# Optimization experiments

Measured on AMD Instinct MI355X. Metric: run time of the kernel, lower is better.

Reference implementation:

```python
import jax, jax.numpy as jnp
import numpy as np
from jax import lax

B_, L_ = 2, 512
D_MODEL, EXPAND, HEAD_DIM, NGROUPS, D_STATE, D_CONV = 512, 2, 64, 1, 64, 3
D_INNER = EXPAND * D_MODEL            # 1024
NHEADS = D_INNER // HEAD_DIM          # 16
CONV_DIM = D_INNER + 2 * NGROUPS * D_STATE   # 1152
D_IN_PROJ = 2 * D_INNER + 2 * NGROUPS * D_STATE + NHEADS  # 2192
RMS_EPS = 1e-5


def silu(x):
    return x * jax.nn.sigmoid(x)


def segsum(x):
    # x: (..., T) -> (..., T, T); out[..., i, j] = sum_{j<k<=i} x[..., k], -inf above diag
    T = x.shape[-1]
    xr = jnp.broadcast_to(x[..., None], x.shape + (T,))
    keep = jnp.tril(jnp.ones((T, T), dtype=bool), -1)
    xr = jnp.where(keep, xr, 0.0)
    s = jnp.cumsum(xr, axis=-2)
    diag = jnp.tril(jnp.ones((T, T), dtype=bool), 0)
    return jnp.where(diag, s, -jnp.inf)


def ssd(x, A, Bm, Cm, chunk):
    # x: (b,l,h,p), A: (b,l,h), Bm/Cm: (b,l,g,n); chunk==1 as in the source forward
    b, l, h, p = x.shape
    c = l // chunk
    n = Bm.shape[-1]
    x = x.reshape(b, c, chunk, h, p)
    Bm = Bm.reshape(b, c, chunk, Bm.shape[2], n)
    Cm = Cm.reshape(b, c, chunk, Cm.shape[2], n)
    A = A.reshape(b, c, chunk, h).transpose(0, 3, 1, 2)        # (b,h,c,l)
    A_cumsum = jnp.cumsum(A, axis=-1)
    Lmat = jnp.exp(segsum(A))                                   # (b,h,c,l,l)
    # broadcast group dim (g==1) to heads, matching torch.einsum broadcasting
    Bb = jnp.broadcast_to(Bm, (b, c, chunk, h, n))
    Cb = jnp.broadcast_to(Cm, (b, c, chunk, h, n))
    Y_diag = jnp.einsum('bclhn,bcshn,bhcls,bcshp->bclhp', Cb, Bb, Lmat, x)
    decay_states = jnp.exp(A_cumsum[:, :, :, -1:] - A_cumsum)   # (b,h,c,l)
    states = jnp.einsum('bclhn,bhcl,bclhp->bchpn', Bb, decay_states, x)
    states = jnp.concatenate([jnp.zeros_like(states[:, :1]), states], axis=1)  # (b,c+1,h,p,n)
    A_last = jnp.pad(A_cumsum[:, :, :, -1], ((0, 0), (0, 0), (1, 0)))          # (b,h,c+1)
    decay_chunk = jnp.exp(segsum(A_last))                       # (b,h,c+1,c+1)
    new_states = jnp.einsum('bhzc,bchpn->bzhpn', decay_chunk, states)
    states = new_states[:, :-1]                                 # (b,c,h,p,n)
    state_decay_out = jnp.exp(A_cumsum)
    Y_off = jnp.einsum('bclhn,bchpn,bhcl->bclhp', Cb, states, state_decay_out)
    return (Y_diag + Y_off).reshape(b, l, h, p)


def causal_dwconv(x, w, bias):
    # x: (B,L,C); w: (C,K) depthwise; torch pads (K-1) both sides then slices [:L] == left-pad only
    xt = x.transpose(0, 2, 1)
    y = lax.conv_general_dilated(xt, w[:, None, :], (1,), [(D_CONV - 1, 0)],
                                 feature_group_count=CONV_DIM,
                                 dimension_numbers=('NCH', 'OIH', 'NCH'))
    return y.transpose(0, 2, 1) + bias


def setup_inputs() -> dict:
    key = jax.random.key(0)
    ks = jax.random.split(key, 8)
    u = jax.random.normal(ks[0], (B_, L_, D_MODEL), dtype=jnp.float32)
    W_in = jax.random.normal(ks[1], (D_MODEL, D_IN_PROJ), dtype=jnp.float32) / np.sqrt(D_MODEL).astype(np.float32)
    conv_w = jax.random.normal(ks[2], (CONV_DIM, D_CONV), dtype=jnp.float32) * 0.3
    conv_b = jnp.zeros((CONV_DIM,), dtype=jnp.float32)
    dt = jnp.exp(jax.random.uniform(ks[3], (NHEADS,), dtype=jnp.float32)
                 * (np.float32(np.log(0.1)) - np.float32(np.log(0.001))) + np.float32(np.log(0.001)))
    dt = jnp.clip(dt, 1e-4, None)
    dt_bias = dt + jnp.log(-jnp.expm1(-dt))
    A_log = jnp.log(jax.random.uniform(ks[4], (NHEADS,), dtype=jnp.float32, minval=1.0, maxval=16.0))
    D_param = jnp.ones((NHEADS,), dtype=jnp.float32)
    rms_w = jnp.ones((D_INNER,), dtype=jnp.float32)
    W_out = jax.random.normal(ks[5], (D_INNER, D_MODEL), dtype=jnp.float32) / np.sqrt(D_INNER).astype(np.float32)
    return {"u": u, "W_in": W_in, "conv_w": conv_w, "conv_b": conv_b, "dt_bias": dt_bias,
            "A_log": A_log, "D_param": D_param, "rms_w": rms_w, "W_out": W_out}


def reference(u, W_in, conv_w, conv_b, dt_bias, A_log, D_param, rms_w, W_out):
    b, l, _ = u.shape
    zxbcdt = u @ W_in                                   # (b,l,D_IN_PROJ)
    z = zxbcdt[..., :D_INNER]
    xBC = zxbcdt[..., D_INNER:D_INNER + CONV_DIM]
    dt = zxbcdt[..., D_INNER + CONV_DIM:]
    dt = jax.nn.softplus(dt + dt_bias)                  # (b,l,h)
    A = -jnp.exp(A_log)                                 # (h,)
    xBC = silu(causal_dwconv(xBC, conv_w, conv_b))      # (b,l,CONV_DIM)
    x = xBC[..., :D_INNER].reshape(b, l, NHEADS, HEAD_DIM)
    Bm = xBC[..., D_INNER:D_INNER + D_STATE][:, :, None, :]     # (b,l,1,n)
    Cm = xBC[..., D_INNER + D_STATE:][:, :, None, :]            # (b,l,1,n)
    y = ssd(x * dt[..., None], A * dt, Bm, Cm, 1)       # (b,l,h,p)
    y = y + x * D_param[:, None]
    y = y.reshape(b, l, D_INNER)
    # gated RMSNorm
    yz = y * silu(z)
    y = yz * lax.rsqrt(jnp.mean(yz * yz, axis=-1, keepdims=True) + RMS_EPS) * rms_w
    return y @ W_out
```

## Files before the change

kernel.cpp:

```cpp
#include <hip/hip_runtime.h>
#include <hip/hip_bf16.h>

#define B_SZ 2
#define L_SZ 512
#define D_MODEL 512
#define D_INNER 1024
#define HEAD_DIM 64
#define NHEADS 16
#define D_STATE 64
#define D_CONV 3
#define CONV_DIM 1152
#define D_IN_PROJ 2192
#define BL (B_SZ * L_SZ)
#define RMS_EPS 1e-5f
#define QC 64
#define NCH 8
#define NPAD1 2304
#define PB 72

typedef __attribute__((ext_vector_type(8))) short short8t;
typedef __attribute__((ext_vector_type(8))) unsigned short ushort8t;
typedef __attribute__((ext_vector_type(4))) unsigned short ushort4t;
typedef __attribute__((ext_vector_type(4))) float f32x4;

__device__ __forceinline__ unsigned short f2bf(float f) {
    unsigned u = __float_as_uint(f);
    u += 0x7fff + ((u >> 16) & 1);
    return (unsigned short)(u >> 16);
}
__device__ __forceinline__ float bf2f(unsigned short u) {
    return __uint_as_float(((unsigned)u) << 16);
}

__device__ __forceinline__ void gload_lds16(const void* g, void* lds) {
    __builtin_amdgcn_global_load_lds(
        (const __attribute__((address_space(1))) unsigned int*)g,
        (__attribute__((address_space(3))) unsigned int*)lds, 16, 0, 0);
}

__device__ __forceinline__ void transpose_tile_bf16(const float* __restrict__ src,
                                                    const float* __restrict__ scale,
                                                    unsigned short* __restrict__ dst,
                                                    int K, int Nin, int tile, int ntn) {
    __shared__ float T[64][65];
    int tid = threadIdx.x;
    int nt = tile % ntn, kt = tile / ntn;
    int n0 = nt * 64, k0 = kt * 64;
#pragma unroll
    for (int rr = 0; rr < 4; ++rr) {
        int k = k0 + (tid >> 4) + rr * 16;
        float sc = scale ? scale[k] : 1.f;
        int nn = (tid & 15) * 4;
#pragma unroll
        for (int q = 0; q < 4; ++q) {
            int n = n0 + nn + q;
            T[(tid >> 4) + rr * 16][nn + q] = (n < Nin) ? src[(size_t)k * Nin + n] * sc : 0.f;
        }
    }
    __syncthreads();
    int nn2 = tid >> 2, kc = tid & 3;
    unsigned short ov[16];
#pragma unroll
    for (int j = 0; j < 16; ++j) ov[j] = f2bf(T[kc * 16 + j][nn2]);
    unsigned short* p = dst + (size_t)(n0 + nn2) * K + k0 + kc * 16;
    *(ushort8t*)p = *(ushort8t*)&ov[0];
    *(ushort8t*)(p + 8) = *(ushort8t*)&ov[8];
}

__global__ __launch_bounds__(256) void prep_kernel(const float* __restrict__ W_in,
                                                   const float* __restrict__ W_out,
                                                   const float* __restrict__ rms_w,
                                                   const float* __restrict__ u,
                                                   unsigned short* __restrict__ Wt1,
                                                   unsigned short* __restrict__ Wt2,
                                                   unsigned short* __restrict__ u_bf) {
    int bid = blockIdx.x;
    if (bid < 288) {
        transpose_tile_bf16(W_in, nullptr, Wt1, D_MODEL, D_IN_PROJ, bid, 36);
    } else if (bid < 416) {
        transpose_tile_bf16(W_out, rms_w, Wt2, D_INNER, D_MODEL, bid - 288, 8);
    } else {
        int i = ((bid - 416) * 256 + threadIdx.x) * 8;
        float4 v0 = *(const float4*)(u + i);
        float4 v1 = *(const float4*)(u + i + 4);
        unsigned short ov[8] = {f2bf(v0.x), f2bf(v0.y), f2bf(v0.z), f2bf(v0.w),
                                f2bf(v1.x), f2bf(v1.y), f2bf(v1.z), f2bf(v1.w)};
        *(ushort8t*)(u_bf + i) = *(ushort8t*)&ov[0];
    }
}

__global__ __launch_bounds__(256) void gemm_in(const unsigned short* __restrict__ A,
                                               const unsigned short* __restrict__ Bt,
                                               unsigned short* __restrict__ z_bf,
                                               unsigned short* __restrict__ xbc,
                                               float* __restrict__ dtb) {
    const int K = D_MODEL;
    __shared__ char sm[49152];
    int tid = threadIdx.x;
    int w = tid >> 6, l = tid & 63;
    int m0 = blockIdx.y * 64, n0 = blockIdx.x * 64;
    int wm = w >> 1, wn = w & 1;

    f32x4 acc[2][2];
#pragma unroll
    for (int i = 0; i < 2; ++i)
#pragma unroll
        for (int j = 0; j < 2; ++j) acc[i][j] = (f32x4){0.f, 0.f, 0.f, 0.f};

    auto stage = [&](const unsigned short* src, int row0, int k0, char* dst) {
#pragma unroll
        for (int p = 0; p < 2; ++p) {
            int c = w * 2 + p;
            int row = c * 8 + (l >> 3);
            int scb = ((l & 7) << 4) ^ ((row & 7) << 4);
            gload_lds16(src + (size_t)(row0 + row) * K + k0 + (scb >> 1), dst + c * 1024);
        }
    };

    const int nkt = K / 64;
    stage(A, m0, 0, sm);
    stage(Bt, n0, 0, sm + 8192);
    stage(A, m0, 64, sm + 16384);
    stage(Bt, n0, 64, sm + 16384 + 8192);

    for (int kt = 0; kt < nkt; ++kt) {
        if (kt + 2 < nkt) {
            char* d = sm + ((kt + 2) % 3) * 16384;
            stage(A, m0, (kt + 2) * 64, d);
            stage(Bt, n0, (kt + 2) * 64, d + 8192);
        }
        int inflight = nkt - 1 - kt;
        if (inflight >= 2)      asm volatile("s_waitcnt vmcnt(8)" ::: "memory");
        else if (inflight == 1) asm volatile("s_waitcnt vmcnt(4)" ::: "memory");
        else                    asm volatile("s_waitcnt vmcnt(0)" ::: "memory");
        __builtin_amdgcn_s_barrier();

        const char* Ab = sm + (kt % 3) * 16384;
        const char* Bb = Ab + 8192;
#pragma unroll
        for (int kk = 0; kk < 2; ++kk) {
            short8t af[2], bf[2];
#pragma unroll
            for (int i = 0; i < 2; ++i) {
                int r = wm * 32 + i * 16 + (l & 15);
                int cb = (kk * 64 + (l >> 4) * 16) ^ ((r & 7) << 4);
                af[i] = *(const short8t*)(Ab + r * 128 + cb);
            }
#pragma unroll
            for (int j = 0; j < 2; ++j) {
                int r = wn * 32 + j * 16 + (l & 15);
                int cb = (kk * 64 + (l >> 4) * 16) ^ ((r & 7) << 4);
                bf[j] = *(const short8t*)(Bb + r * 128 + cb);
            }
#pragma unroll
            for (int i = 0; i < 2; ++i)
#pragma unroll
                for (int j = 0; j < 2; ++j)
                    acc[i][j] = __builtin_amdgcn_mfma_f32_16x16x32_bf16(af[i], bf[j], acc[i][j], 0, 0, 0);
        }
        __builtin_amdgcn_s_barrier();
    }

#pragma unroll
    for (int i = 0; i < 2; ++i)
#pragma unroll
        for (int j = 0; j < 2; ++j) {
            int row = m0 + wm * 32 + i * 16 + (l >> 4) * 4;
            int col = n0 + wn * 32 + j * 16 + (l & 15);
#pragma unroll
            for (int r = 0; r < 4; ++r) {
                float v = acc[i][j][r];
                int rr = row + r;
                if (col < D_INNER) {
                    z_bf[(size_t)rr * D_INNER + col] = f2bf(v);
                } else if (col < D_INNER + CONV_DIM) {
                    xbc[(size_t)rr * CONV_DIM + (col - D_INNER)] = f2bf(v);
                } else if (col < D_IN_PROJ) {
                    dtb[(size_t)rr * 16 + (col - D_INNER - CONV_DIM)] = v;
                }
            }
        }
}

__device__ __forceinline__ float4 conv4b(const unsigned short* __restrict__ xrow,
                                         int gl, int ch,
                                         const float* __restrict__ conv_w,
                                         const float* __restrict__ conv_b) {
    ushort4t u2 = *(const ushort4t*)(xrow + ch);
    ushort4t u1 = {0, 0, 0, 0}, u0 = {0, 0, 0, 0};
    if (gl >= 1) u1 = *(const ushort4t*)(xrow + ch - CONV_DIM);
    if (gl >= 2) u0 = *(const ushort4t*)(xrow + ch - 2 * CONV_DIM);
    float4 o;
    float a;
    a = conv_b[ch+0] + conv_w[(ch+0)*3]*bf2f(u0[0]) + conv_w[(ch+0)*3+1]*bf2f(u1[0]) + conv_w[(ch+0)*3+2]*bf2f(u2[0]);
    o.x = a / (1.f + __expf(-a));
    a = conv_b[ch+1] + conv_w[(ch+1)*3]*bf2f(u0[1]) + conv_w[(ch+1)*3+1]*bf2f(u1[1]) + conv_w[(ch+1)*3+2]*bf2f(u2[1]);
    o.y = a / (1.f + __expf(-a));
    a = conv_b[ch+2] + conv_w[(ch+2)*3]*bf2f(u0[2]) + conv_w[(ch+2)*3+1]*bf2f(u1[2]) + conv_w[(ch+2)*3+2]*bf2f(u2[2]);
    o.z = a / (1.f + __expf(-a));
    a = conv_b[ch+3] + conv_w[(ch+3)*3]*bf2f(u0[3]) + conv_w[(ch+3)*3+1]*bf2f(u1[3]) + conv_w[(ch+3)*3+2]*bf2f(u2[3]);
    o.w = a / (1.f + __expf(-a));
    return o;
}

__device__ __forceinline__ float silu(float z) { return z / (1.f + __expf(-z)); }

__global__ __launch_bounds__(256) void ssd_passA(const unsigned short* __restrict__ xbc,
                                                 const float* __restrict__ dtb,
                                                 const unsigned short* __restrict__ z_bf,
                                                 const float* __restrict__ conv_w,
                                                 const float* __restrict__ conv_b,
                                                 const float* __restrict__ dt_bias,
                                                 const float* __restrict__ A_log,
                                                 const float* __restrict__ D_param,
                                                 unsigned short* __restrict__ y_bf,
                                                 unsigned short* __restrict__ yz_bf,
                                                 float* __restrict__ psum,
                                                 unsigned short* __restrict__ Zbuf,
                                                 float* __restrict__ Ebuf) {
    int blk = blockIdx.x;
    int h = blk & 15;
    int c = (blk >> 4) & 7;
    int b = blk >> 7;
    int tid = threadIdx.x;

    __shared__ __align__(16) unsigned short Cs_bf[QC][PB];
    __shared__ __align__(16) unsigned short Bs_bf[QC][PB];
    __shared__ __align__(16) unsigned short XDT_bf[QC][PB];
    __shared__ __align__(16) unsigned short BTw_bf[QC][PB];
    __shared__ float csh[QC], dts[QC], wh[QC];
    __shared__ float sq_lds[QC][2];
#define PS_bf Cs_bf

    int bl0 = b * L_SZ + c * QC;

    if (tid < 64) {
        int t = tid;
        float draw = dtb[(size_t)(bl0 + t) * 16 + h];
        float dtv = draw + dt_bias[h];
        dtv = (dtv > 20.f) ? dtv : log1pf(expf(dtv));
        float A = -expf(A_log[h]);
        float cs = A * dtv;
#pragma unroll
        for (int off = 1; off < 64; off <<= 1) {
            float tmp = __shfl_up(cs, off);
            if (t >= off) cs += tmp;
        }
        float cs63 = __shfl(cs, 63);
        dts[t] = dtv;
        csh[t] = cs;
        wh[t] = __expf(cs63 - cs);
        Ebuf[(((size_t)(b * NHEADS + h) * NCH) + c) * QC + t] = __expf(cs);
    }

    int row16 = tid >> 4;
    int col4 = (tid & 15) * 4;
#pragma unroll
    for (int r = 0; r < 4; ++r) {
        int t = r * 16 + row16;
        int gl = c * QC + t;
        const unsigned short* xrow = xbc + (size_t)(bl0 + t) * CONV_DIM;
        float4 Bv = conv4b(xrow, gl, D_INNER + col4, conv_w, conv_b);
        float4 Cv = conv4b(xrow, gl, D_INNER + D_STATE + col4, conv_w, conv_b);
        ushort4t bq = {f2bf(Bv.x), f2bf(Bv.y), f2bf(Bv.z), f2bf(Bv.w)};
        ushort4t cq = {f2bf(Cv.x), f2bf(Cv.y), f2bf(Cv.z), f2bf(Cv.w)};
        *(ushort4t*)&Bs_bf[t][col4] = bq;
        *(ushort4t*)&Cs_bf[t][col4] = cq;
    }
    __syncthreads();

#pragma unroll
    for (int r = 0; r < 4; ++r) {
        int t = r * 16 + row16;
        int gl = c * QC + t;
        const unsigned short* xrow = xbc + (size_t)(bl0 + t) * CONV_DIM;
        float4 xv = conv4b(xrow, gl, h * HEAD_DIM + col4, conv_w, conv_b);
        float d = dts[t], wt = wh[t];
        xv.x *= d; xv.y *= d; xv.z *= d; xv.w *= d;
        ushort4t xq = {f2bf(xv.x), f2bf(xv.y), f2bf(xv.z), f2bf(xv.w)};
        ushort4t bq = *(ushort4t*)&Bs_bf[t][col4];
#pragma unroll
        for (int q = 0; q < 4; ++q) {
            int ch = col4 + q;
            int f8 = ((ch >> 2) & 7) << 3;
            XDT_bf[ch][t ^ f8] = xq[q];
            BTw_bf[ch][t ^ f8] = f2bf(bf2f(bq[q]) * wt);
        }
    }
    __syncthreads();

    int l = tid & 63, wv = tid >> 6;
    int wm = wv >> 1, wn = wv & 1;
    int fr = l & 15, fq = l >> 4;

    f32x4 g[2][2];
    {
#pragma unroll
        for (int i = 0; i < 2; ++i)
#pragma unroll
            for (int j = 0; j < 2; ++j) g[i][j] = (f32x4){0.f, 0.f, 0.f, 0.f};
#pragma unroll
        for (int kk = 0; kk < 2; ++kk) {
            short8t af[2], bb[2];
#pragma unroll
            for (int i = 0; i < 2; ++i)
                af[i] = *(const short8t*)&Cs_bf[wm * 32 + i * 16 + fr][kk * 32 + fq * 8];
#pragma unroll
            for (int j = 0; j < 2; ++j)
                bb[j] = *(const short8t*)&Bs_bf[wn * 32 + j * 16 + fr][kk * 32 + fq * 8];
#pragma unroll
            for (int i = 0; i < 2; ++i)
#pragma unroll
                for (int j = 0; j < 2; ++j)
                    g[i][j] = __builtin_amdgcn_mfma_f32_16x16x32_bf16(af[i], bb[j], g[i][j], 0, 0, 0);
        }
    }
    __syncthreads();

    {
#pragma unroll
        for (int i = 0; i < 2; ++i)
#pragma unroll
            for (int j = 0; j < 2; ++j) {
                int s = wn * 32 + j * 16 + fr;
                float css = csh[s];
#pragma unroll
                for (int r = 0; r < 4; ++r) {
                    int t = wm * 32 + i * 16 + fq * 4 + r;
                    float v = (s <= t) ? g[i][j][r] * __expf(csh[t] - css) : 0.f;
                    PS_bf[t][s] = f2bf(v);
                }
            }
    }
    __syncthreads();

    {
        f32x4 yv[2][2];
#pragma unroll
        for (int i = 0; i < 2; ++i)
#pragma unroll
            for (int j = 0; j < 2; ++j) yv[i][j] = (f32x4){0.f, 0.f, 0.f, 0.f};
#pragma unroll
        for (int kk = 0; kk < 2; ++kk) {
            short8t af[2], bb[2];
            int K0 = kk * 32 + fq * 8;
#pragma unroll
            for (int i = 0; i < 2; ++i)
                af[i] = *(const short8t*)&PS_bf[wm * 32 + i * 16 + fr][K0];
#pragma unroll
            for (int j = 0; j < 2; ++j) {
                int r = wn * 32 + j * 16 + fr;
                bb[j] = *(const short8t*)&XDT_bf[r][K0 ^ (((r >> 2) & 7) << 3)];
            }
#pragma unroll
            for (int i = 0; i < 2; ++i)
#pragma unroll
                for (int j = 0; j < 2; ++j)
                    yv[i][j] = __builtin_amdgcn_mfma_f32_16x16x32_bf16(af[i], bb[j], yv[i][j], 0, 0, 0);
        }
        float Dp = D_param[h];
        if (c == 0) {
            float sloc[2][4] = {{0.f, 0.f, 0.f, 0.f}, {0.f, 0.f, 0.f, 0.f}};
#pragma unroll
            for (int i = 0; i < 2; ++i)
#pragma unroll
                for (int j = 0; j < 2; ++j) {
                    int p = wn * 32 + j * 16 + fr;
                    int f8 = ((p >> 2) & 7) << 3;
#pragma unroll
                    for (int r = 0; r < 4; ++r) {
                        int t = wm * 32 + i * 16 + fq * 4 + r;
                        float xval = bf2f(XDT_bf[p][t ^ f8]);
                        float yval = yv[i][j][r] + (Dp / dts[t]) * xval;
                        float z = bf2f(z_bf[(size_t)(bl0 + t) * D_INNER + h * HEAD_DIM + p]);
                        float yz = yval * silu(z);
                        yz_bf[(size_t)(bl0 + t) * D_INNER + h * HEAD_DIM + p] = f2bf(yz);
                        sloc[i][r] += yz * yz;
                    }
                }
#pragma unroll
            for (int i = 0; i < 2; ++i)
#pragma unroll
                for (int r = 0; r < 4; ++r) {
                    float v = sloc[i][r];
                    v += __shfl_xor(v, 1); v += __shfl_xor(v, 2);
                    v += __shfl_xor(v, 4); v += __shfl_xor(v, 8);
                    if (fr == 0) {
                        int t = wm * 32 + i * 16 + fq * 4 + r;
                        sq_lds[t][wn] = v;
                    }
                }
            __syncthreads();
            if (tid < 64)
                psum[(size_t)(bl0 + tid) * 16 + h] = sq_lds[tid][0] + sq_lds[tid][1];
        } else {
#pragma unroll
            for (int i = 0; i < 2; ++i)
#pragma unroll
                for (int j = 0; j < 2; ++j) {
                    int p = wn * 32 + j * 16 + fr;
                    int f8 = ((p >> 2) & 7) << 3;
#pragma unroll
                    for (int r = 0; r < 4; ++r) {
                        int t = wm * 32 + i * 16 + fq * 4 + r;
                        float xval = bf2f(XDT_bf[p][t ^ f8]);
                        float fct = Dp / dts[t];
                        y_bf[(size_t)(bl0 + t) * D_INNER + h * HEAD_DIM + p] =
                            f2bf(yv[i][j][r] + fct * xval);
                    }
                }
        }
    }

    {
        f32x4 zv[2][2];
#pragma unroll
        for (int i = 0; i < 2; ++i)
#pragma unroll
            for (int j = 0; j < 2; ++j) zv[i][j] = (f32x4){0.f, 0.f, 0.f, 0.f};
#pragma unroll
        for (int kk = 0; kk < 2; ++kk) {
            short8t af[2], bb[2];
            int K0 = kk * 32 + fq * 8;
#pragma unroll
            for (int i = 0; i < 2; ++i) {
                int r = wm * 32 + i * 16 + fr;
                af[i] = *(const short8t*)&XDT_bf[r][K0 ^ (((r >> 2) & 7) << 3)];
            }
#pragma unroll
            for (int j = 0; j < 2; ++j) {
                int r = wn * 32 + j * 16 + fr;
                bb[j] = *(const short8t*)&BTw_bf[r][K0 ^ (((r >> 2) & 7) << 3)];
            }
#pragma unroll
            for (int i = 0; i < 2; ++i)
#pragma unroll
                for (int j = 0; j < 2; ++j)
                    zv[i][j] = __builtin_amdgcn_mfma_f32_16x16x32_bf16(af[i], bb[j], zv[i][j], 0, 0, 0);
        }
        unsigned short* Zr = Zbuf + (((size_t)(b * NHEADS + h) * NCH) + c) * (HEAD_DIM * D_STATE);
#pragma unroll
        for (int i = 0; i < 2; ++i)
#pragma unroll
            for (int j = 0; j < 2; ++j) {
                int n = wn * 32 + j * 16 + fr;
#pragma unroll
                for (int r = 0; r < 4; ++r) {
                    int p = wm * 32 + i * 16 + fq * 4 + r;
                    Zr[p * D_STATE + n] = f2bf(zv[i][j][r]);
                }
            }
    }
#undef PS_bf
}

__global__ __launch_bounds__(256) void ssd_passC(const unsigned short* __restrict__ xbc,
                                                 const unsigned short* __restrict__ z_bf,
                                                 const float* __restrict__ conv_w,
                                                 const float* __restrict__ conv_b,
                                                 const unsigned short* __restrict__ Zbuf,
                                                 const float* __restrict__ Ebuf,
                                                 const unsigned short* __restrict__ y_bf,
                                                 unsigned short* __restrict__ yz_bf,
                                                 float* __restrict__ psum) {
    int blk = blockIdx.x;
    int h = blk & 15;
    int q = blk >> 4;
    int c = 1 + (q % 7);
    int b = q / 7;
    int tid = threadIdx.x;

    __shared__ __align__(16) unsigned short Cs_bf[QC][PB];
    __shared__ __align__(16) unsigned short S_bf[QC][PB];
    __shared__ float Eh[QC];
    __shared__ float sq_lds[QC][2];

    int bl0 = b * L_SZ + c * QC;
    const unsigned short* Zb = Zbuf + ((size_t)(b * NHEADS + h) * NCH) * (HEAD_DIM * D_STATE);
    const float* Eb = Ebuf + ((size_t)(b * NHEADS + h) * NCH) * QC;

    {
        int p = tid >> 2, nq = (tid & 3) * 16;
        float S16[16];
#pragma unroll
        for (int qq = 0; qq < 16; ++qq) S16[qq] = 0.f;
        float wgt = 1.f;
        for (int j = c - 1; j >= 0; --j) {
            const unsigned short* Zj = Zb + (size_t)j * (HEAD_DIM * D_STATE) + p * D_STATE + nq;
            ushort8t za = *(const ushort8t*)Zj;
            ushort8t zb2 = *(const ushort8t*)(Zj + 8);
#pragma unroll
            for (int qq = 0; qq < 8; ++qq) {
                S16[qq] += wgt * bf2f(za[qq]);
                S16[8 + qq] += wgt * bf2f(zb2[qq]);
            }
            wgt *= Eb[(size_t)j * QC + 63];
        }
#pragma unroll
        for (int q4 = 0; q4 < 4; ++q4) {
            ushort4t s4 = {f2bf(S16[q4 * 4 + 0]), f2bf(S16[q4 * 4 + 1]),
                           f2bf(S16[q4 * 4 + 2]), f2bf(S16[q4 * 4 + 3])};
            *(ushort4t*)&S_bf[p][nq + q4 * 4] = s4;
        }
    }

    int row16 = tid >> 4, col4 = (tid & 15) * 4;
#pragma unroll
    for (int r = 0; r < 4; ++r) {
        int t = r * 16 + row16;
        int gl = c * QC + t;
        const unsigned short* xrow = xbc + (size_t)(bl0 + t) * CONV_DIM;
        float4 Cv = conv4b(xrow, gl, D_INNER + D_STATE + col4, conv_w, conv_b);
        ushort4t cq = {f2bf(Cv.x), f2bf(Cv.y), f2bf(Cv.z), f2bf(Cv.w)};
        *(ushort4t*)&Cs_bf[t][col4] = cq;
    }
    if (tid < 64)
        Eh[tid] = Ebuf[(((size_t)(b * NHEADS + h) * NCH) + c) * QC + tid];
    __syncthreads();

    int l = tid & 63, wv = tid >> 6;
    int wm = wv >> 1, wn = wv & 1;
    int fr = l & 15, fq = l >> 4;
    f32x4 acc[2][2];
#pragma unroll
    for (int i = 0; i < 2; ++i)
#pragma unroll
        for (int j = 0; j < 2; ++j) acc[i][j] = (f32x4){0.f, 0.f, 0.f, 0.f};
#pragma unroll
    for (int kk = 0; kk < 2; ++kk) {
        short8t af[2], bb[2];
#pragma unroll
        for (int i = 0; i < 2; ++i)
            af[i] = *(const short8t*)&Cs_bf[wm * 32 + i * 16 + fr][kk * 32 + fq * 8];
#pragma unroll
        for (int j = 0; j < 2; ++j)
            bb[j] = *(const short8t*)&S_bf[wn * 32 + j * 16 + fr][kk * 32 + fq * 8];
#pragma unroll
        for (int i = 0; i < 2; ++i)
#pragma unroll
            for (int j = 0; j < 2; ++j)
                acc[i][j] = __builtin_amdgcn_mfma_f32_16x16x32_bf16(af[i], bb[j], acc[i][j], 0, 0, 0);
    }

    float sloc[2][4] = {{0.f, 0.f, 0.f, 0.f}, {0.f, 0.f, 0.f, 0.f}};
#pragma unroll
    for (int i = 0; i < 2; ++i)
#pragma unroll
        for (int j = 0; j < 2; ++j) {
            int p = wn * 32 + j * 16 + fr;
#pragma unroll
            for (int r = 0; r < 4; ++r) {
                int t = wm * 32 + i * 16 + fq * 4 + r;
                size_t idx = (size_t)(bl0 + t) * D_INNER + h * HEAD_DIM + p;
                float yval = bf2f(y_bf[idx]) + Eh[t] * acc[i][j][r];
                float z = bf2f(z_bf[idx]);
                float yz = yval * silu(z);
                yz_bf[idx] = f2bf(yz);
                sloc[i][r] += yz * yz;
            }
        }
#pragma unroll
    for (int i = 0; i < 2; ++i)
#pragma unroll
        for (int r = 0; r < 4; ++r) {
            float v = sloc[i][r];
            v += __shfl_xor(v, 1); v += __shfl_xor(v, 2);
            v += __shfl_xor(v, 4); v += __shfl_xor(v, 8);
            if (fr == 0) {
                int t = wm * 32 + i * 16 + fq * 4 + r;
                sq_lds[t][wn] = v;
            }
        }
    __syncthreads();
    if (tid < 64)
        psum[(size_t)(bl0 + tid) * 16 + h] = sq_lds[tid][0] + sq_lds[tid][1];
}

__global__ __launch_bounds__(256) void gemm_out(const unsigned short* __restrict__ A,
                                                const unsigned short* __restrict__ Bt,
                                                const float* __restrict__ psum,
                                                float* __restrict__ C) {
    const int N = D_MODEL, K = D_INNER;
    __shared__ char sm[36864];
    __shared__ float scl[32];
    int tid = threadIdx.x;
    int w = tid >> 6, l = tid & 63;
    int m0 = blockIdx.y * 32, n0 = blockIdx.x * 64;
    int wm = w >> 1, wn = w & 1;

    f32x4 acc[2];
    acc[0] = (f32x4){0.f, 0.f, 0.f, 0.f};
    acc[1] = (f32x4){0.f, 0.f, 0.f, 0.f};

    auto stageA = [&](int k0, char* dst) {
        int row = w * 8 + (l >> 3);
        int scb = ((l & 7) << 4) ^ ((row & 7) << 4);
        gload_lds16(A + (size_t)(m0 + row) * K + k0 + (scb >> 1), dst + w * 1024);
    };
    auto stageB = [&](int k0, char* dst) {
#pragma unroll
        for (int p = 0; p < 2; ++p) {
            int c = w * 2 + p;
            int row = c * 8 + (l >> 3);
            int scb = ((l & 7) << 4) ^ ((row & 7) << 4);
            gload_lds16(Bt + (size_t)(n0 + row) * K + k0 + (scb >> 1), dst + c * 1024);
        }
    };

    const int nkt = K / 64;
    stageA(0, sm); stageB(0, sm + 4096);
    stageA(64, sm + 12288); stageB(64, sm + 12288 + 4096);

    for (int kt = 0; kt < nkt; ++kt) {
        if (kt + 2 < nkt) {
            char* d = sm + ((kt + 2) % 3) * 12288;
            stageA((kt + 2) * 64, d);
            stageB((kt + 2) * 64, d + 4096);
        }
        int inflight = nkt - 1 - kt;
        if (inflight >= 2)      asm volatile("s_waitcnt vmcnt(6)" ::: "memory");
        else if (inflight == 1) asm volatile("s_waitcnt vmcnt(3)" ::: "memory");
        else                    asm volatile("s_waitcnt vmcnt(0)" ::: "memory");
        __builtin_amdgcn_s_barrier();

        const char* Ab = sm + (kt % 3) * 12288;
        const char* Bb = Ab + 4096;
#pragma unroll
        for (int kk = 0; kk < 2; ++kk) {
            short8t af;
            {
                int r = wm * 16 + (l & 15);
                int cb = (kk * 64 + (l >> 4) * 16) ^ ((r & 7) << 4);
                af = *(const short8t*)(Ab + r * 128 + cb);
            }
#pragma unroll
            for (int j = 0; j < 2; ++j) {
                int r = wn * 32 + j * 16 + (l & 15);
                int cb = (kk * 64 + (l >> 4) * 16) ^ ((r & 7) << 4);
                short8t bfv = *(const short8t*)(Bb + r * 128 + cb);
                acc[j] = __builtin_amdgcn_mfma_f32_16x16x32_bf16(af, bfv, acc[j], 0, 0, 0);
            }
        }
        __builtin_amdgcn_s_barrier();
    }

    if (tid < 32) {
        const float* pr = psum + (size_t)(m0 + tid) * 16;
        float s = 0.f;
#pragma unroll
        for (int qq = 0; qq < 16; ++qq) s += pr[qq];
        scl[tid] = rsqrtf(s / (float)D_INNER + RMS_EPS);
    }
    __syncthreads();

#pragma unroll
    for (int j = 0; j < 2; ++j) {
        int col = n0 + wn * 32 + j * 16 + (l & 15);
        int rloc = wm * 16 + (l >> 4) * 4;
#pragma unroll
        for (int r = 0; r < 4; ++r)
            C[(size_t)(m0 + rloc + r) * N + col] = acc[j][r] * scl[rloc + r];
    }
}

extern "C" void kernel_launch(void* const* d_in, const int* in_sizes, int n_in,
                              void* d_out, int out_size, void* d_ws, size_t ws_size,
                              hipStream_t stream) {
    const float* u       = (const float*)d_in[0];
    const float* W_in    = (const float*)d_in[1];
    const float* conv_w  = (const float*)d_in[2];
    const float* conv_b  = (const float*)d_in[3];
    const float* dt_bias = (const float*)d_in[4];
    const float* A_log   = (const float*)d_in[5];
    const float* D_param = (const float*)d_in[6];
    const float* rms_w   = (const float*)d_in[7];
    const float* W_out   = (const float*)d_in[8];
    float* out = (float*)d_out;

    float* ws = (float*)d_ws;
    float* Ebuf = ws;
    float* dtb  = Ebuf + (size_t)32 * NCH * QC;
    float* psum = dtb + (size_t)BL * 16;
    unsigned short* u_bf  = (unsigned short*)(psum + (size_t)BL * 16);
    unsigned short* Wt1   = u_bf + (size_t)BL * D_MODEL;
    unsigned short* Wt2   = Wt1 + (size_t)NPAD1 * D_MODEL;
    unsigned short* xbc   = Wt2 + (size_t)D_MODEL * D_INNER;
    unsigned short* z_bf  = xbc + (size_t)BL * CONV_DIM;
    unsigned short* y_bf  = z_bf + (size_t)BL * D_INNER;
    unsigned short* yz_bf = y_bf + (size_t)BL * D_INNER;
    unsigned short* Zbuf  = yz_bf + (size_t)BL * D_INNER;

    prep_kernel<<<672, 256, 0, stream>>>(W_in, W_out, rms_w, u, Wt1, Wt2, u_bf);

    gemm_in<<<dim3(NPAD1 / 64, BL / 64), 256, 0, stream>>>(
        u_bf, Wt1, z_bf, xbc, dtb);

    ssd_passA<<<B_SZ * NCH * NHEADS, 256, 0, stream>>>(
        xbc, dtb, z_bf, conv_w, conv_b, dt_bias, A_log, D_param,
        y_bf, yz_bf, psum, Zbuf, Ebuf);
    ssd_passC<<<224, 256, 0, stream>>>(
        xbc, z_bf, conv_w, conv_b, Zbuf, Ebuf, y_bf, yz_bf, psum);

    gemm_out<<<dim3(D_MODEL / 64, BL / 32), 256, 0, stream>>>(
        yz_bf, Wt2, psum, out);
}
```

Before: 46.25 us.

## Fuse SSD passes into one kernel with inter-block flag synchronization

Merges ssd_passA and ssd_passC into a single kernel. Each chunk block publishes its chunk state (Zbuf) and chunk decay, then sets a release flag. Later chunks spin on acquire flags of earlier chunks and add the inter-chunk contribution directly in registers. This removes a kernel launch, the y_bf round trip through global memory and the recomputed B/C conv in passC. The cost is a spin-wait dependency that assumes all 256 blocks are co-resident and serializes later chunks behind earlier ones.

```diff
diff --git a/kernel.cpp b/kernel.cpp
--- a/kernel.cpp
+++ b/kernel.cpp
@@ -73,8 +73,10 @@
                                                    const float* __restrict__ u,
                                                    unsigned short* __restrict__ Wt1,
                                                    unsigned short* __restrict__ Wt2,
-                                                   unsigned short* __restrict__ u_bf) {
+                                                   unsigned short* __restrict__ u_bf,
+                                                   unsigned* __restrict__ flags) {
     int bid = blockIdx.x;
+    if (bid == 0) flags[threadIdx.x] = 0u;
     if (bid < 288) {
         transpose_tile_bf16(W_in, nullptr, Wt1, D_MODEL, D_IN_PROJ, bid, 36);
     } else if (bid < 416) {
@@ -205,7 +207,7 @@
 
 __device__ __forceinline__ float silu(float z) { return z / (1.f + __expf(-z)); }
 
-__global__ __launch_bounds__(256) void ssd_passA(const unsigned short* __restrict__ xbc,
+__global__ __launch_bounds__(256) void ssd_fused(const unsigned short* __restrict__ xbc,
                                                  const float* __restrict__ dtb,
                                                  const unsigned short* __restrict__ z_bf,
                                                  const float* __restrict__ conv_w,
@@ -213,15 +215,16 @@
                                                  const float* __restrict__ dt_bias,
                                                  const float* __restrict__ A_log,
                                                  const float* __restrict__ D_param,
-                                                 unsigned short* __restrict__ y_bf,
                                                  unsigned short* __restrict__ yz_bf,
                                                  float* __restrict__ psum,
                                                  unsigned short* __restrict__ Zbuf,
-                                                 float* __restrict__ Ebuf) {
+                                                 float* __restrict__ dec,
+                                                 unsigned* __restrict__ flags) {
     int blk = blockIdx.x;
     int h = blk & 15;
     int c = (blk >> 4) & 7;
     int b = blk >> 7;
+    int bh = b * NHEADS + h;
     int tid = threadIdx.x;
 
     __shared__ __align__(16) unsigned short Cs_bf[QC][PB];
@@ -230,7 +233,8 @@
     __shared__ __align__(16) unsigned short BTw_bf[QC][PB];
     __shared__ float csh[QC], dts[QC], wh[QC];
     __shared__ float sq_lds[QC][2];
-#define PS_bf Cs_bf
+#define P_bf Bs_bf
+#define S_bf BTw_bf
 
     int bl0 = b * L_SZ + c * QC;
 
@@ -250,7 +254,7 @@
         dts[t] = dtv;
         csh[t] = cs;
         wh[t] = __expf(cs63 - cs);
-        Ebuf[(((size_t)(b * NHEADS + h) * NCH) + c) * QC + t] = __expf(cs);
+        if (t == 0) dec[bh * NCH + c] = __expf(cs63);
     }
 
     int row16 = tid >> 4;
@@ -294,135 +298,77 @@
     int fr = l & 15, fq = l >> 4;
 
     f32x4 g[2][2];
+#pragma unroll
+    for (int i = 0; i < 2; ++i)
+#pragma unroll
+        for (int j = 0; j < 2; ++j) g[i][j] = (f32x4){0.f, 0.f, 0.f, 0.f};
+#pragma unroll
+    for (int kk = 0; kk < 2; ++kk) {
+        short8t af[2], bb[2];
+#pragma unroll
+        for (int i = 0; i < 2; ++i)
+            af[i] = *(const short8t*)&Cs_bf[wm * 32 + i * 16 + fr][kk * 32 + fq * 8];
+#pragma unroll
+        for (int j = 0; j < 2; ++j)
+            bb[j] = *(const short8t*)&Bs_bf[wn * 32 + j * 16 + fr][kk * 32 + fq * 8];
+#pragma unroll
+        for (int i = 0; i < 2; ++i)
+#pragma unroll
+            for (int j = 0; j < 2; ++j)
+                g[i][j] = __builtin_amdgcn_mfma_f32_16x16x32_bf16(af[i], bb[j], g[i][j], 0, 0, 0);
+    }
+    __syncthreads();
+
+#pragma unroll
+    for (int i = 0; i < 2; ++i)
+#pragma unroll
+        for (int j = 0; j < 2; ++j) {
+            int s = wn * 32 + j * 16 + fr;
+            float css = csh[s];
+#pragma unroll
+            for (int r = 0; r < 4; ++r) {
+                int t = wm * 32 + i * 16 + fq * 4 + r;
+                float v = (s <= t) ? g[i][j][r] * __expf(csh[t] - css) : 0.f;
+                P_bf[t][s] = f2bf(v);
+            }
+        }
+    __syncthreads();
+
+    f32x4 yv[2][2];
+#pragma unroll
+    for (int i = 0; i < 2; ++i)
+#pragma unroll
+        for (int j = 0; j < 2; ++j) yv[i][j] = (f32x4){0.f, 0.f, 0.f, 0.f};
+#pragma unroll
+    for (int kk = 0; kk < 2; ++kk) {
+        short8t af[2], bb[2];
+        int K0 = kk * 32 + fq * 8;
+#pragma unroll
+        for (int i = 0; i < 2; ++i)
+            af[i] = *(const short8t*)&P_bf[wm * 32 + i * 16 + fr][K0];
+#pragma unroll
+        for (int j = 0; j < 2; ++j) {
+            int r = wn * 32 + j * 16 + fr;
+            bb[j] = *(const short8t*)&XDT_bf[r][K0 ^ (((r >> 2) & 7) << 3)];
+        }
+#pragma unroll
+        for (int i = 0; i < 2; ++i)
+#pragma unroll
+            for (int j = 0; j < 2; ++j)
+                yv[i][j] = __builtin_amdgcn_mfma_f32_16x16x32_bf16(af[i], bb[j], yv[i][j], 0, 0, 0);
+    }
+
     {
-#pragma unroll
-        for (int i = 0; i < 2; ++i)
-#pragma unroll
-            for (int j = 0; j < 2; ++j) g[i][j] = (f32x4){0.f, 0.f, 0.f, 0.f};
-#pragma unroll
-        for (int kk = 0; kk < 2; ++kk) {
-            short8t af[2], bb[2];
-#pragma unroll
-            for (int i = 0; i < 2; ++i)
-                af[i] = *(const short8t*)&Cs_bf[wm * 32 + i * 16 + fr][kk * 32 + fq * 8];
-#pragma unroll
-            for (int j = 0; j < 2; ++j)
-                bb[j] = *(const short8t*)&Bs_bf[wn * 32 + j * 16 + fr][kk * 32 + fq * 8];
-#pragma unroll
-            for (int i = 0; i < 2; ++i)
-#pragma unroll
-                for (int j = 0; j < 2; ++j)
-                    g[i][j] = __builtin_amdgcn_mfma_f32_16x16x32_bf16(af[i], bb[j], g[i][j], 0, 0, 0);
-        }
-    }
-    __syncthreads();
-
-    {
-#pragma unroll
-        for (int i = 0; i < 2; ++i)
-#pragma unroll
-            for (int j = 0; j < 2; ++j) {
-                int s = wn * 32 + j * 16 + fr;
-                float css = csh[s];
-#pragma unroll
-                for (int r = 0; r < 4; ++r) {
-                    int t = wm * 32 + i * 16 + fq * 4 + r;
-                    float v = (s <= t) ? g[i][j][r] * __expf(csh[t] - css) : 0.f;
-                    PS_bf[t][s] = f2bf(v);
-                }
-            }
-    }
-    __syncthreads();
-
-    {
-        f32x4 yv[2][2];
-#pragma unroll
-        for (int i = 0; i < 2; ++i)
-#pragma unroll
-            for (int j = 0; j < 2; ++j) yv[i][j] = (f32x4){0.f, 0.f, 0.f, 0.f};
+        f32x4 zv[2][2];
+#pragma unroll
+        for (int i = 0; i < 2; ++i)
+#pragma unroll
+            for (int j = 0; j < 2; ++j) zv[i][j] = (f32x4){0.f, 0.f, 0.f, 0.f};
 #pragma unroll
         for (int kk = 0; kk < 2; ++kk) {
             short8t af[2], bb[2];
             int K0 = kk * 32 + fq * 8;
 #pragma unroll
-            for (int i = 0; i < 2; ++i)
-                af[i] = *(const short8t*)&PS_bf[wm * 32 + i * 16 + fr][K0];
-#pragma unroll
-            for (int j = 0; j < 2; ++j) {
-                int r = wn * 32 + j * 16 + fr;
-                bb[j] = *(const short8t*)&XDT_bf[r][K0 ^ (((r >> 2) & 7) << 3)];
-            }
-#pragma unroll
-            for (int i = 0; i < 2; ++i)
-#pragma unroll
-                for (int j = 0; j < 2; ++j)
-                    yv[i][j] = __builtin_amdgcn_mfma_f32_16x16x32_bf16(af[i], bb[j], yv[i][j], 0, 0, 0);
-        }
-        float Dp = D_param[h];
-        if (c == 0) {
-            float sloc[2][4] = {{0.f, 0.f, 0.f, 0.f}, {0.f, 0.f, 0.f, 0.f}};
-#pragma unroll
-            for (int i = 0; i < 2; ++i)
-#pragma unroll
-                for (int j = 0; j < 2; ++j) {
-                    int p = wn * 32 + j * 16 + fr;
-                    int f8 = ((p >> 2) & 7) << 3;
-#pragma unroll
-                    for (int r = 0; r < 4; ++r) {
-                        int t = wm * 32 + i * 16 + fq * 4 + r;
-                        float xval = bf2f(XDT_bf[p][t ^ f8]);
-                        float yval = yv[i][j][r] + (Dp / dts[t]) * xval;
-                        float z = bf2f(z_bf[(size_t)(bl0 + t) * D_INNER + h * HEAD_DIM + p]);
-                        float yz = yval * silu(z);
-                        yz_bf[(size_t)(bl0 + t) * D_INNER + h * HEAD_DIM + p] = f2bf(yz);
-                        sloc[i][r] += yz * yz;
-                    }
-                }
-#pragma unroll
-            for (int i = 0; i < 2; ++i)
-#pragma unroll
-                for (int r = 0; r < 4; ++r) {
-                    float v = sloc[i][r];
-                    v += __shfl_xor(v, 1); v += __shfl_xor(v, 2);
-                    v += __shfl_xor(v, 4); v += __shfl_xor(v, 8);
-                    if (fr == 0) {
-                        int t = wm * 32 + i * 16 + fq * 4 + r;
-                        sq_lds[t][wn] = v;
-                    }
-                }
-            __syncthreads();
-            if (tid < 64)
-                psum[(size_t)(bl0 + tid) * 16 + h] = sq_lds[tid][0] + sq_lds[tid][1];
-        } else {
-#pragma unroll
-            for (int i = 0; i < 2; ++i)
-#pragma unroll
-                for (int j = 0; j < 2; ++j) {
-                    int p = wn * 32 + j * 16 + fr;
-                    int f8 = ((p >> 2) & 7) << 3;
-#pragma unroll
-                    for (int r = 0; r < 4; ++r) {
-                        int t = wm * 32 + i * 16 + fq * 4 + r;
-                        float xval = bf2f(XDT_bf[p][t ^ f8]);
-                        float fct = Dp / dts[t];
-                        y_bf[(size_t)(bl0 + t) * D_INNER + h * HEAD_DIM + p] =
-                            f2bf(yv[i][j][r] + fct * xval);
-                    }
-                }
-        }
-    }
-
-    {
-        f32x4 zv[2][2];
-#pragma unroll
-        for (int i = 0; i < 2; ++i)
-#pragma unroll
-            for (int j = 0; j < 2; ++j) zv[i][j] = (f32x4){0.f, 0.f, 0.f, 0.f};
-#pragma unroll
-        for (int kk = 0; kk < 2; ++kk) {
-            short8t af[2], bb[2];
-            int K0 = kk * 32 + fq * 8;
-#pragma unroll
             for (int i = 0; i < 2; ++i) {
                 int r = wm * 32 + i * 16 + fr;
                 af[i] = *(const short8t*)&XDT_bf[r][K0 ^ (((r >> 2) & 7) << 3)];
@@ -438,7 +384,7 @@
                 for (int j = 0; j < 2; ++j)
                     zv[i][j] = __builtin_amdgcn_mfma_f32_16x16x32_bf16(af[i], bb[j], zv[i][j], 0, 0, 0);
         }
-        unsigned short* Zr = Zbuf + (((size_t)(b * NHEADS + h) * NCH) + c) * (HEAD_DIM * D_STATE);
+        unsigned short* Zr = Zbuf + (((size_t)bh * NCH) + c) * (HEAD_DIM * D_STATE);
 #pragma unroll
         for (int i = 0; i < 2; ++i)
 #pragma unroll
@@ -451,129 +397,117 @@
                 }
             }
     }
-#undef PS_bf
-}
-
-__global__ __launch_bounds__(256) void ssd_passC(const unsigned short* __restrict__ xbc,
-                                                 const unsigned short* __restrict__ z_bf,
-                                                 const float* __restrict__ conv_w,
-                                                 const float* __restrict__ conv_b,
-                                                 const unsigned short* __restrict__ Zbuf,
-                                                 const float* __restrict__ Ebuf,
-                                                 const unsigned short* __restrict__ y_bf,
-                                                 unsigned short* __restrict__ yz_bf,
-                                                 float* __restrict__ psum) {
-    int blk = blockIdx.x;
-    int h = blk & 15;
-    int q = blk >> 4;
-    int c = 1 + (q % 7);
-    int b = q / 7;
-    int tid = threadIdx.x;
-
-    __shared__ __align__(16) unsigned short Cs_bf[QC][PB];
-    __shared__ __align__(16) unsigned short S_bf[QC][PB];
-    __shared__ float Eh[QC];
-    __shared__ float sq_lds[QC][2];
-
-    int bl0 = b * L_SZ + c * QC;
-    const unsigned short* Zb = Zbuf + ((size_t)(b * NHEADS + h) * NCH) * (HEAD_DIM * D_STATE);
-    const float* Eb = Ebuf + ((size_t)(b * NHEADS + h) * NCH) * QC;
+    asm volatile("s_waitcnt vmcnt(0)" ::: "memory");
+    __syncthreads();
+    if (tid == 0)
+        __hip_atomic_store(&flags[bh * NCH + c], 1u, __ATOMIC_RELEASE, __HIP_MEMORY_SCOPE_AGENT);
+
+    if (c > 0) {
+        if (tid == 0) {
+            for (int j = 0; j < c; ++j)
+                while (__hip_atomic_load(&flags[bh * NCH + j], __ATOMIC_ACQUIRE,
+                                         __HIP_MEMORY_SCOPE_AGENT) == 0u)
+                    __builtin_amdgcn_s_sleep(8);
+        }
+        __syncthreads();
+
+        {
+            int p = tid >> 2, nq = (tid & 3) * 16;
+            const unsigned short* Zb = Zbuf + ((size_t)bh * NCH) * (HEAD_DIM * D_STATE);
+            float S16[16];
+#pragma unroll
+            for (int qq = 0; qq < 16; ++qq) S16[qq] = 0.f;
+            float wgt = 1.f;
+            for (int j = c - 1; j >= 0; --j) {
+                const unsigned short* Zj = Zb + (size_t)j * (HEAD_DIM * D_STATE) + p * D_STATE + nq;
+                ushort8t za = *(const ushort8t*)Zj;
+                ushort8t zb2 = *(const ushort8t*)(Zj + 8);
+#pragma unroll
+                for (int qq = 0; qq < 8; ++qq) {
+                    S16[qq] += wgt * bf2f(za[qq]);
+                    S16[8 + qq] += wgt * bf2f(zb2[qq]);
+                }
+                wgt *= dec[bh * NCH + j];
+            }
+#pragma unroll
+            for (int q4 = 0; q4 < 4; ++q4) {
+                ushort4t s4 = {f2bf(S16[q4 * 4 + 0]), f2bf(S16[q4 * 4 + 1]),
+                               f2bf(S16[q4 * 4 + 2]), f2bf(S16[q4 * 4 + 3])};
+                *(ushort4t*)&S_bf[p][nq + q4 * 4] = s4;
+            }
+        }
+        __syncthreads();
+
+        f32x4 acc[2][2];
+#pragma unroll
+        for (int i = 0; i < 2; ++i)
+#pragma unroll
+            for (int j = 0; j < 2; ++j) acc[i][j] = (f32x4){0.f, 0.f, 0.f, 0.f};
+#pragma unroll
+        for (int kk = 0; kk < 2; ++kk) {
+            short8t af[2], bb[2];
+#pragma unroll
+            for (int i = 0; i < 2; ++i)
+                af[i] = *(const short8t*)&Cs_bf[wm * 32 + i * 16 + fr][kk * 32 + fq * 8];
+#pragma unroll
+            for (int j = 0; j < 2; ++j)
+                bb[j] = *(const short8t*)&S_bf[wn * 32 + j * 16 + fr][kk * 32 + fq * 8];
+#pragma unroll
+            for (int i = 0; i < 2; ++i)
+#pragma unroll
+                for (int j = 0; j < 2; ++j)
+                    acc[i][j] = __builtin_amdgcn_mfma_f32_16x16x32_bf16(af[i], bb[j], acc[i][j], 0, 0, 0);
+        }
+#pragma unroll
+        for (int i = 0; i < 2; ++i)
+#pragma unroll
+            for (int j = 0; j < 2; ++j)
+#pragma unroll
+                for (int r = 0; r < 4; ++r) {
+                    int t = wm * 32 + i * 16 + fq * 4 + r;
+                    yv[i][j][r] += __expf(csh[t]) * acc[i][j][r];
+                }
+    }
 
     {
-        int p = tid >> 2, nq = (tid & 3) * 16;
-        float S16[16];
-#pragma unroll
-        for (int qq = 0; qq < 16; ++qq) S16[qq] = 0.f;
-        float wgt = 1.f;
-        for (int j = c - 1; j >= 0; --j) {
-            const unsigned short* Zj = Zb + (size_t)j * (HEAD_DIM * D_STATE) + p * D_STATE + nq;
-            ushort8t za = *(const ushort8t*)Zj;
-            ushort8t zb2 = *(const ushort8t*)(Zj + 8);
-#pragma unroll
-            for (int qq = 0; qq < 8; ++qq) {
-                S16[qq] += wgt * bf2f(za[qq]);
-                S16[8 + qq] += wgt * bf2f(zb2[qq]);
-            }
-            wgt *= Eb[(size_t)j * QC + 63];
-        }
-#pragma unroll
-        for (int q4 = 0; q4 < 4; ++q4) {
-            ushort4t s4 = {f2bf(S16[q4 * 4 + 0]), f2bf(S16[q4 * 4 + 1]),
-                           f2bf(S16[q4 * 4 + 2]), f2bf(S16[q4 * 4 + 3])};
-            *(ushort4t*)&S_bf[p][nq + q4 * 4] = s4;
-        }
-    }
-
-    int row16 = tid >> 4, col4 = (tid & 15) * 4;
-#pragma unroll
-    for (int r = 0; r < 4; ++r) {
-        int t = r * 16 + row16;
-        int gl = c * QC + t;
-        const unsigned short* xrow = xbc + (size_t)(bl0 + t) * CONV_DIM;
-        float4 Cv = conv4b(xrow, gl, D_INNER + D_STATE + col4, conv_w, conv_b);
-        ushort4t cq = {f2bf(Cv.x), f2bf(Cv.y), f2bf(Cv.z), f2bf(Cv.w)};
-        *(ushort4t*)&Cs_bf[t][col4] = cq;
-    }
-    if (tid < 64)
-        Eh[tid] = Ebuf[(((size_t)(b * NHEADS + h) * NCH) + c) * QC + tid];
-    __syncthreads();
-
-    int l = tid & 63, wv = tid >> 6;
-    int wm = wv >> 1, wn = wv & 1;
-    int fr = l & 15, fq = l >> 4;
-    f32x4 acc[2][2];
-#pragma unroll
-    for (int i = 0; i < 2; ++i)
-#pragma unroll
-        for (int j = 0; j < 2; ++j) acc[i][j] = (f32x4){0.f, 0.f, 0.f, 0.f};
-#pragma unroll
-    for (int kk = 0; kk < 2; ++kk) {
-        short8t af[2], bb[2];
-#pragma unroll
-        for (int i = 0; i < 2; ++i)
-            af[i] = *(const short8t*)&Cs_bf[wm * 32 + i * 16 + fr][kk * 32 + fq * 8];
-#pragma unroll
-        for (int j = 0; j < 2; ++j)
-            bb[j] = *(const short8t*)&S_bf[wn * 32 + j * 16 + fr][kk * 32 + fq * 8];
-#pragma unroll
-        for (int i = 0; i < 2; ++i)
-#pragma unroll
-            for (int j = 0; j < 2; ++j)
-                acc[i][j] = __builtin_amdgcn_mfma_f32_16x16x32_bf16(af[i], bb[j], acc[i][j], 0, 0, 0);
-    }
-
-    float sloc[2][4] = {{0.f, 0.f, 0.f, 0.f}, {0.f, 0.f, 0.f, 0.f}};
-#pragma unroll
-    for (int i = 0; i < 2; ++i)
-#pragma unroll
-        for (int j = 0; j < 2; ++j) {
-            int p = wn * 32 + j * 16 + fr;
+        float Dp = D_param[h];
+        float sloc[2][4] = {{0.f, 0.f, 0.f, 0.f}, {0.f, 0.f, 0.f, 0.f}};
+#pragma unroll
+        for (int i = 0; i < 2; ++i)
+#pragma unroll
+            for (int j = 0; j < 2; ++j) {
+                int p = wn * 32 + j * 16 + fr;
+                int f8 = ((p >> 2) & 7) << 3;
+#pragma unroll
+                for (int r = 0; r < 4; ++r) {
+                    int t = wm * 32 + i * 16 + fq * 4 + r;
+                    float xval = bf2f(XDT_bf[p][t ^ f8]);
+                    float yval = yv[i][j][r] + (Dp / dts[t]) * xval;
+                    size_t idx = (size_t)(bl0 + t) * D_INNER + h * HEAD_DIM + p;
+                    float z = bf2f(z_bf[idx]);
+                    float yz = yval * silu(z);
+                    yz_bf[idx] = f2bf(yz);
+                    sloc[i][r] += yz * yz;
+                }
+            }
+#pragma unroll
+        for (int i = 0; i < 2; ++i)
 #pragma unroll
             for (int r = 0; r < 4; ++r) {
-                int t = wm * 32 + i * 16 + fq * 4 + r;
-                size_t idx = (size_t)(bl0 + t) * D_INNER + h * HEAD_DIM + p;
-                float yval = bf2f(y_bf[idx]) + Eh[t] * acc[i][j][r];
-                float z = bf2f(z_bf[idx]);
-                float yz = yval * silu(z);
-                yz_bf[idx] = f2bf(yz);
-                sloc[i][r] += yz * yz;
-            }
-        }
-#pragma unroll
-    for (int i = 0; i < 2; ++i)
-#pragma unroll
-        for (int r = 0; r < 4; ++r) {
-            float v = sloc[i][r];
-            v += __shfl_xor(v, 1); v += __shfl_xor(v, 2);
-            v += __shfl_xor(v, 4); v += __shfl_xor(v, 8);
-            if (fr == 0) {
-                int t = wm * 32 + i * 16 + fq * 4 + r;
-                sq_lds[t][wn] = v;
-            }
-        }
-    __syncthreads();
-    if (tid < 64)
-        psum[(size_t)(bl0 + tid) * 16 + h] = sq_lds[tid][0] + sq_lds[tid][1];
+                float v = sloc[i][r];
+                v += __shfl_xor(v, 1); v += __shfl_xor(v, 2);
+                v += __shfl_xor(v, 4); v += __shfl_xor(v, 8);
+                if (fr == 0) {
+                    int t = wm * 32 + i * 16 + fq * 4 + r;
+                    sq_lds[t][wn] = v;
+                }
+            }
+        __syncthreads();
+        if (tid < 64)
+            psum[(size_t)(bl0 + tid) * 16 + h] = sq_lds[tid][0] + sq_lds[tid][1];
+    }
+#undef P_bf
+#undef S_bf
 }
 
 __global__ __launch_bounds__(256) void gemm_out(const unsigned short* __restrict__ A,
@@ -678,28 +612,26 @@
     float* out = (float*)d_out;
 
     float* ws = (float*)d_ws;
-    float* Ebuf = ws;
-    float* dtb  = Ebuf + (size_t)32 * NCH * QC;
+    float* dec  = ws;
+    float* dtb  = dec + 256;
     float* psum = dtb + (size_t)BL * 16;
-    unsigned short* u_bf  = (unsigned short*)(psum + (size_t)BL * 16);
+    unsigned* flags = (unsigned*)(psum + (size_t)BL * 16);
+    unsigned short* u_bf  = (unsigned short*)(flags + 256);
     unsigned short* Wt1   = u_bf + (size_t)BL * D_MODEL;
     unsigned short* Wt2   = Wt1 + (size_t)NPAD1 * D_MODEL;
     unsigned short* xbc   = Wt2 + (size_t)D_MODEL * D_INNER;
     unsigned short* z_bf  = xbc + (size_t)BL * CONV_DIM;
-    unsigned short* y_bf  = z_bf + (size_t)BL * D_INNER;
-    unsigned short* yz_bf = y_bf + (size_t)BL * D_INNER;
+    unsigned short* yz_bf = z_bf + (size_t)BL * D_INNER;
     unsigned short* Zbuf  = yz_bf + (size_t)BL * D_INNER;
 
-    prep_kernel<<<672, 256, 0, stream>>>(W_in, W_out, rms_w, u, Wt1, Wt2, u_bf);
+    prep_kernel<<<672, 256, 0, stream>>>(W_in, W_out, rms_w, u, Wt1, Wt2, u_bf, flags);
 
     gemm_in<<<dim3(NPAD1 / 64, BL / 64), 256, 0, stream>>>(
         u_bf, Wt1, z_bf, xbc, dtb);
 
-    ssd_passA<<<B_SZ * NCH * NHEADS, 256, 0, stream>>>(
+    ssd_fused<<<B_SZ * NCH * NHEADS, 256, 0, stream>>>(
         xbc, dtb, z_bf, conv_w, conv_b, dt_bias, A_log, D_param,
-        y_bf, yz_bf, psum, Zbuf, Ebuf);
-    ssd_passC<<<224, 256, 0, stream>>>(
-        xbc, z_bf, conv_w, conv_b, Zbuf, Ebuf, y_bf, yz_bf, psum);
+        yz_bf, psum, Zbuf, dec, flags);
 
     gemm_out<<<dim3(D_MODEL / 64, BL / 32), 256, 0, stream>>>(
         yz_bf, Wt2, psum, out);
```

Result: slower. 54.99 us (+18.9%).
